# Performance work log

Hardware: AMD Instinct MI355X
Metric: run time of the kernel (lower is better)

Reference implementation:

```python
import jax, jax.numpy as jnp
import numpy as np

KSIZE = 3        # kernel_size
SW = 4           # spatial_groups = (1, 4): blocks along width only
KBITS = 4        # fake-quant bits for the kernel


def fake_quant_weights(w, num_bits=KBITS):
    # per-tensor symmetric fake quant with straight-through estimator
    qmax = float(2 ** (num_bits - 1) - 1)  # 7 for 4 bits
    scale = jnp.max(jnp.abs(w)) / qmax
    q = jnp.round(w / scale) * scale
    return w + jax.lax.stop_gradient(q - w)


def setup_inputs() -> dict:
    key = jax.random.key(0)
    k1, k2 = jax.random.split(key, 2)
    N, C, H, W, F = 32, 64, 56, 56, 128
    inputs = jax.random.normal(k1, (N, C, H, W), dtype=jnp.float32)
    # glorot_uniform over (fan_in = k*k*C, fan_out = F)
    fan_in = KSIZE * KSIZE * C
    limit = float(np.sqrt(6.0 / (fan_in + F)))
    kernel = jax.random.uniform(k2, (1, SW, fan_in, F), dtype=jnp.float32,
                                minval=-limit, maxval=limit)
    bias = jnp.zeros((F,), dtype=jnp.float32)
    return {"inputs": inputs, "kernel": kernel, "bias": bias}


def reference(inputs, kernel, bias):
    # inputs: [N, C, H, W]; kernel: [1, SW, C*K*K, F]; bias: [F]
    N, C, H, W = inputs.shape
    F = kernel.shape[-1]
    qk = fake_quant_weights(kernel, KBITS)[0]          # [SW, C*K*K, F]

    xp = jnp.pad(inputs, ((0, 0), (0, 0), (1, 1), (1, 1)))  # pad H,W by 1
    # im2col: patch flattened over (C, kh, kw), matching K.local_conv NCHW
    # patches: [N, C, K*K, H, W] -> [N, C*K*K, H, W]
    patches = jnp.stack(
        [xp[:, :, i:i + H, j:j + W] for i in range(KSIZE) for j in range(KSIZE)],
        axis=2,
    ).reshape(N, C * KSIZE * KSIZE, H, W)

    # split output columns into SW contiguous blocks of width W//SW,
    # each block uses its own weight matrix (w_interval = (W+2)//SW = W//SW here)
    Wb = W // SW
    p = patches.reshape(N, C * KSIZE * KSIZE, H, SW, Wb)   # [N, P, H, SW, Wb]
    out = jnp.einsum('nphbw,bpf->nfhbw', p, qk)            # [N, F, H, SW, Wb]
    out = out.reshape(N, F, H, W) + bias[None, :, None, None]
    return out
```

## Files before the change

### kernel.cpp

```cpp
#include <hip/hip_runtime.h>
#include <hip/hip_bf16.h>

#define CIN   64
#define HH_   56
#define WW_   56
#define FOUT  128
#define NN    32
#define SW    4
#define WB    14
#define HG    8
#define NHG   7
#define NW    (SW*9*FOUT*CIN)

typedef __attribute__((ext_vector_type(8))) short bf16x8;
typedef __attribute__((ext_vector_type(4))) float f32x4;

__device__ inline unsigned short f2bf(float x) {
    unsigned u = __float_as_uint(x);
    return (unsigned short)((u + 0x7FFFu + ((u >> 16) & 1u)) >> 16);
}

__global__ void absmax_part(const float* __restrict__ w, float* __restrict__ part) {
    __shared__ float sm[4];
    int tid = threadIdx.x;
    float m = 0.f;
    for (int idx = blockIdx.x * 256 + tid; idx < NW; idx += 64 * 256)
        m = fmaxf(m, fabsf(w[idx]));
    #pragma unroll
    for (int off = 32; off > 0; off >>= 1)
        m = fmaxf(m, __shfl_down(m, off, 64));
    if ((tid & 63) == 0) sm[tid >> 6] = m;
    __syncthreads();
    if (tid == 0)
        part[blockIdx.x] = fmaxf(fmaxf(sm[0], sm[1]), fmaxf(sm[2], sm[3]));
}

__global__ void quant_t(const float* __restrict__ w, const float* __restrict__ part,
                        unsigned short* __restrict__ qwt) {
    float pm = part[threadIdx.x & 63];
    #pragma unroll
    for (int off = 1; off < 64; off <<= 1)
        pm = fmaxf(pm, __shfl_xor(pm, off, 64));
    float scale = pm / 7.0f;
    int o = blockIdx.x * 256 + threadIdx.x;
    if (o >= NW) return;
    int ks = o & 63;
    int f  = (o >> 6) & 127;
    int bt = o >> 13;
    int t  = bt - (bt / 9) * 9;
    int b  = bt / 9;
    int c  = ks ^ ((f & 7) << 3);
    float v = w[((b * CIN + c) * 9 + t) * FOUT + f];
    qwt[o] = f2bf(rintf(v / scale) * scale);
}

__global__ __launch_bounds__(256, 3)
void conv_mfma(const float* __restrict__ in,
               const unsigned short* __restrict__ qwt,
               const float* __restrict__ bias,
               float* __restrict__ out) {
    const int hg = blockIdx.x, n = blockIdx.y, b = blockIdx.z;
    const int h0 = hg * HG, w0 = b * WB;
    const int tid = threadIdx.x;
    const int wave = tid >> 6, lane = tid & 63;
    const int q = lane >> 4, lm = lane & 15;
    const int wf = wave >> 1, wp = wave & 1;

    __shared__ __align__(16) unsigned short s_slab[160 * 64];
    __shared__ __align__(16) unsigned short s_w[2][128 * 64];

    for (int e = tid; e < 160 * 64; e += 256) {
        int col = e & 15, c = (e >> 4) & 63, hh = e >> 10;
        int hi = h0 - 1 + hh, wi = w0 - 1 + col;
        float v = 0.f;
        if (hi >= 0 && hi < HH_ && wi >= 0 && wi < WW_)
            v = in[((n * CIN + c) * HH_ + hi) * WW_ + wi];
        int pix = hh * 16 + col;
        s_slab[pix * 64 + (c ^ ((pix & 7) << 3))] = f2bf(v);
    }

    const unsigned short* wsrc = qwt + (size_t)b * 9 * FOUT * CIN;

    #pragma unroll
    for (int i = 0; i < 4; ++i) {
        int off = (i * 256 + tid) * 8;
        __builtin_amdgcn_global_load_lds(
            (const __attribute__((address_space(1))) void*)(wsrc + off),
            (__attribute__((address_space(3))) void*)(&s_w[0][off]), 16, 0, 0);
    }
    __syncthreads();

    f32x4 acc[4][4];
    #pragma unroll
    for (int i = 0; i < 4; ++i)
        #pragma unroll
        for (int j = 0; j < 4; ++j)
            acc[i][j] = (f32x4){0.f, 0.f, 0.f, 0.f};

    for (int t = 0; t < 9; ++t) {
        if (t < 8) {
            const unsigned short* src = wsrc + (size_t)(t + 1) * FOUT * CIN;
            #pragma unroll
            for (int i = 0; i < 4; ++i) {
                int off = (i * 256 + tid) * 8;
                __builtin_amdgcn_global_load_lds(
                    (const __attribute__((address_space(1))) void*)(src + off),
                    (__attribute__((address_space(3))) void*)(&s_w[(t + 1) & 1][off]),
                    16, 0, 0);
            }
        }
        const int kh = t / 3, kw = t - (t / 3) * 3;
        const unsigned short* wb_ = s_w[t & 1];

        #pragma unroll
        for (int cc = 0; cc < 2; ++cc) {
            const int koff = cc * 32 + q * 8;
            bf16x8 af[4], bfr[4];
            #pragma unroll
            for (int m = 0; m < 4; ++m) {
                int f = (wf * 4 + m) * 16 + lm;
                af[m] = *(const bf16x8*)&wb_[f * 64 + (koff ^ ((f & 7) << 3))];
            }
            #pragma unroll
            for (int p = 0; p < 4; ++p) {
                int sp = (wp * 4 + p + kh) * 16 + ((lm + kw) & 15);
                bfr[p] = *(const bf16x8*)&s_slab[sp * 64 + (koff ^ ((sp & 7) << 3))];
            }
            #pragma unroll
            for (int m = 0; m < 4; ++m)
                #pragma unroll
                for (int p = 0; p < 4; ++p)
                    acc[m][p] = __builtin_amdgcn_mfma_f32_16x16x32_bf16(
                        af[m], bfr[p], acc[m][p], 0, 0, 0);
        }
        if (t < 8) __syncthreads();
    }

    #pragma unroll
    for (int m = 0; m < 4; ++m) {
        #pragma unroll
        for (int r = 0; r < 4; ++r) {
            int f = (wf * 4 + m) * 16 + q * 4 + r;
            float bv = bias[f];
            if (lm < WB) {
                #pragma unroll
                for (int p = 0; p < 4; ++p) {
                    int row = wp * 4 + p;
                    out[(((size_t)n * FOUT + f) * HH_ + h0 + row) * WW_ + w0 + lm] =
                        acc[m][p][r] + bv;
                }
            }
        }
    }
}

extern "C" void kernel_launch(void* const* d_in, const int* in_sizes, int n_in,
                              void* d_out, int out_size, void* d_ws, size_t ws_size,
                              hipStream_t stream) {
    const float* inputs = (const float*)d_in[0];
    const float* kernel = (const float*)d_in[1];
    const float* bias   = (const float*)d_in[2];
    float* out          = (float*)d_out;

    float*          part = (float*)d_ws;
    unsigned short* qwt  = (unsigned short*)((char*)d_ws + 512);

    absmax_part<<<64, 256, 0, stream>>>(kernel, part);
    quant_t<<<(NW + 255) / 256, 256, 0, stream>>>(kernel, part, qwt);

    dim3 grid(NHG, NN, SW);
    conv_mfma<<<grid, 256, 0, stream>>>(inputs, qwt, bias, out);
}
```

Before: 136.0 us.

## Hold quantized weights in registers with MFMA-fragment packing and larger row tiles

The quantizer now writes bf16 weights pre-packed in MFMA A-fragment order, so each wave loads its 2×9×2 weight fragments straight from global memory into registers once. The LDS weight double-buffer and the per-tap barriers go away. Blocks grow to 512 threads covering 14 output rows, which cuts the redundant halo rows in the input slab. Slab fill now reads two channels per thread and stores them as packed 32-bit words. In exchange, register pressure rises (36 bf16x8 weight fragments plus 14 accumulators), which may cut occupancy, and the grid shrinks to 4×32×4 blocks.

```diff
diff --git a/kernel.cpp b/kernel.cpp
--- a/kernel.cpp
+++ b/kernel.cpp
@@ -8,9 +8,9 @@
 #define NN    32
 #define SW    4
 #define WB    14
-#define HG    8
-#define NHG   7
+#define HB    14
 #define NW    (SW*9*FOUT*CIN)
+#define QWT_PER_B (8*9*2*64*8)
 
 typedef __attribute__((ext_vector_type(8))) short bf16x8;
 typedef __attribute__((ext_vector_type(4))) float f32x4;
@@ -35,8 +35,8 @@
         part[blockIdx.x] = fmaxf(fmaxf(sm[0], sm[1]), fmaxf(sm[2], sm[3]));
 }
 
-__global__ void quant_t(const float* __restrict__ w, const float* __restrict__ part,
-                        unsigned short* __restrict__ qwt) {
+__global__ void quant_pack(const float* __restrict__ w, const float* __restrict__ part,
+                           unsigned short* __restrict__ qwt) {
     float pm = part[threadIdx.x & 63];
     #pragma unroll
     for (int off = 1; off < 64; off <<= 1)
@@ -44,111 +44,102 @@
     float scale = pm / 7.0f;
     int o = blockIdx.x * 256 + threadIdx.x;
     if (o >= NW) return;
-    int ks = o & 63;
-    int f  = (o >> 6) & 127;
-    int bt = o >> 13;
-    int t  = bt - (bt / 9) * 9;
-    int b  = bt / 9;
-    int c  = ks ^ ((f & 7) << 3);
+    int r    = o & 7;
+    int lane = (o >> 3) & 63;
+    int cc   = (o >> 9) & 1;
+    int idx  = o >> 10;
+    int t    = idx % 9;
+    int ft   = (idx / 9) & 7;
+    int b    = idx / 72;
+    int f = ft * 16 + (lane & 15);
+    int c = cc * 32 + (lane >> 4) * 8 + r;
     float v = w[((b * CIN + c) * 9 + t) * FOUT + f];
     qwt[o] = f2bf(rintf(v / scale) * scale);
 }
 
-__global__ __launch_bounds__(256, 3)
+__global__ __launch_bounds__(512, 2)
 void conv_mfma(const float* __restrict__ in,
                const unsigned short* __restrict__ qwt,
                const float* __restrict__ bias,
                float* __restrict__ out) {
-    const int hg = blockIdx.x, n = blockIdx.y, b = blockIdx.z;
-    const int h0 = hg * HG, w0 = b * WB;
+    const int hgb = blockIdx.x, n = blockIdx.y, b = blockIdx.z;
+    const int h0 = hgb * HB, w0 = b * WB;
     const int tid = threadIdx.x;
     const int wave = tid >> 6, lane = tid & 63;
     const int q = lane >> 4, lm = lane & 15;
     const int wf = wave >> 1, wp = wave & 1;
 
-    __shared__ __align__(16) unsigned short s_slab[160 * 64];
-    __shared__ __align__(16) unsigned short s_w[2][128 * 64];
+    __shared__ __align__(16) unsigned short s_slab[256 * 64];
 
-    for (int e = tid; e < 160 * 64; e += 256) {
-        int col = e & 15, c = (e >> 4) & 63, hh = e >> 10;
-        int hi = h0 - 1 + hh, wi = w0 - 1 + col;
-        float v = 0.f;
-        if (hi >= 0 && hi < HH_ && wi >= 0 && wi < WW_)
-            v = in[((n * CIN + c) * HH_ + hi) * WW_ + wi];
-        int pix = hh * 16 + col;
-        s_slab[pix * 64 + (c ^ ((pix & 7) << 3))] = f2bf(v);
-    }
-
-    const unsigned short* wsrc = qwt + (size_t)b * 9 * FOUT * CIN;
+    const unsigned short* wbase = qwt + (size_t)b * QWT_PER_B + lane * 8;
+    bf16x8 wt[2][9][2];
+    #pragma unroll
+    for (int m = 0; m < 2; ++m)
+        #pragma unroll
+        for (int t = 0; t < 9; ++t)
+            #pragma unroll
+            for (int cc = 0; cc < 2; ++cc)
+                wt[m][t][cc] = *(const bf16x8*)&wbase[((((wf * 2 + m) * 9) + t) * 2 + cc) * 512];
 
     #pragma unroll
-    for (int i = 0; i < 4; ++i) {
-        int off = (i * 256 + tid) * 8;
-        __builtin_amdgcn_global_load_lds(
-            (const __attribute__((address_space(1))) void*)(wsrc + off),
-            (__attribute__((address_space(3))) void*)(&s_w[0][off]), 16, 0, 0);
+    for (int i = 0; i < 16; ++i) {
+        int e = i * 512 + tid;
+        int cp  = e & 15;
+        int c0  = ((e >> 4) & 31) * 2;
+        int row = e >> 9;
+        int hi = h0 - 1 + row, wi = w0 - 1 + cp;
+        float v0 = 0.f, v1 = 0.f;
+        if (hi >= 0 && hi < HH_ && wi >= 0 && wi < WW_) {
+            const float* p = &in[((n * CIN + c0) * HH_ + hi) * WW_ + wi];
+            v0 = p[0]; v1 = p[HH_ * WW_];
+        }
+        unsigned pk = (unsigned)f2bf(v0) | ((unsigned)f2bf(v1) << 16);
+        int pix = row * 16 + cp;
+        *(unsigned*)&s_slab[pix * 64 + (c0 ^ ((cp & 7) << 3))] = pk;
     }
     __syncthreads();
 
-    f32x4 acc[4][4];
+    f32x4 acc[2][7];
     #pragma unroll
-    for (int i = 0; i < 4; ++i)
+    for (int m = 0; m < 2; ++m)
         #pragma unroll
-        for (int j = 0; j < 4; ++j)
-            acc[i][j] = (f32x4){0.f, 0.f, 0.f, 0.f};
+        for (int p = 0; p < 7; ++p)
+            acc[m][p] = (f32x4){0.f, 0.f, 0.f, 0.f};
 
+    #pragma unroll
     for (int t = 0; t < 9; ++t) {
-        if (t < 8) {
-            const unsigned short* src = wsrc + (size_t)(t + 1) * FOUT * CIN;
-            #pragma unroll
-            for (int i = 0; i < 4; ++i) {
-                int off = (i * 256 + tid) * 8;
-                __builtin_amdgcn_global_load_lds(
-                    (const __attribute__((address_space(1))) void*)(src + off),
-                    (__attribute__((address_space(3))) void*)(&s_w[(t + 1) & 1][off]),
-                    16, 0, 0);
-            }
-        }
         const int kh = t / 3, kw = t - (t / 3) * 3;
-        const unsigned short* wb_ = s_w[t & 1];
-
+        const int sc  = (lm + kw) & 15;
+        const int swz = (sc & 7) << 3;
         #pragma unroll
         for (int cc = 0; cc < 2; ++cc) {
             const int koff = cc * 32 + q * 8;
-            bf16x8 af[4], bfr[4];
+            bf16x8 bfr[7];
             #pragma unroll
-            for (int m = 0; m < 4; ++m) {
-                int f = (wf * 4 + m) * 16 + lm;
-                af[m] = *(const bf16x8*)&wb_[f * 64 + (koff ^ ((f & 7) << 3))];
+            for (int p = 0; p < 7; ++p) {
+                int srow = wp * 7 + p + kh;
+                bfr[p] = *(const bf16x8*)&s_slab[(srow * 16 + sc) * 64 + (koff ^ swz)];
             }
             #pragma unroll
-            for (int p = 0; p < 4; ++p) {
-                int sp = (wp * 4 + p + kh) * 16 + ((lm + kw) & 15);
-                bfr[p] = *(const bf16x8*)&s_slab[sp * 64 + (koff ^ ((sp & 7) << 3))];
-            }
-            #pragma unroll
-            for (int m = 0; m < 4; ++m)
+            for (int m = 0; m < 2; ++m)
                 #pragma unroll
-                for (int p = 0; p < 4; ++p)
+                for (int p = 0; p < 7; ++p)
                     acc[m][p] = __builtin_amdgcn_mfma_f32_16x16x32_bf16(
-                        af[m], bfr[p], acc[m][p], 0, 0, 0);
+                        wt[m][t][cc], bfr[p], acc[m][p], 0, 0, 0);
         }
-        if (t < 8) __syncthreads();
     }
 
-    #pragma unroll
-    for (int m = 0; m < 4; ++m) {
+    if (lm < WB) {
         #pragma unroll
-        for (int r = 0; r < 4; ++r) {
-            int f = (wf * 4 + m) * 16 + q * 4 + r;
-            float bv = bias[f];
-            if (lm < WB) {
+        for (int m = 0; m < 2; ++m) {
+            #pragma unroll
+            for (int r = 0; r < 4; ++r) {
+                int f = (wf * 2 + m) * 16 + q * 4 + r;
+                float bv = bias[f];
+                float* op = &out[(((size_t)n * FOUT + f) * HH_ + h0 + wp * 7) * WW_ + w0 + lm];
                 #pragma unroll
-                for (int p = 0; p < 4; ++p) {
-                    int row = wp * 4 + p;
-                    out[(((size_t)n * FOUT + f) * HH_ + h0 + row) * WW_ + w0 + lm] =
-                        acc[m][p][r] + bv;
-                }
+                for (int p = 0; p < 7; ++p)
+                    op[p * WW_] = acc[m][p][r] + bv;
             }
         }
     }
@@ -166,8 +157,8 @@
     unsigned short* qwt  = (unsigned short*)((char*)d_ws + 512);
 
     absmax_part<<<64, 256, 0, stream>>>(kernel, part);
-    quant_t<<<(NW + 255) / 256, 256, 0, stream>>>(kernel, part, qwt);
+    quant_pack<<<(NW + 255) / 256, 256, 0, stream>>>(kernel, part, qwt);
 
-    dim3 grid(NHG, NN, SW);
-    conv_mfma<<<grid, 256, 0, stream>>>(inputs, qwt, bias, out);
+    dim3 grid(HH_ / HB, NN, SW);
+    conv_mfma<<<grid, 512, 0, stream>>>(inputs, qwt, bias, out);
 }
```

After: 117.9 us. 13.3% less time.
